# Kernel tuning notes

Measured on AMD Instinct MI355X. Metric: run time of the kernel, lower is better.

The kernel has to match this reference:

```python
import jax, jax.numpy as jnp
import numpy as np

DEPTH = 9                 # complete binary tree depth
N = 2 ** (DEPTH + 1) - 1  # 1023 nodes per tree (heap layout)
B = 32                    # batch of trees
E = 256                   # word_emb_dims
H = 512                   # treelstm in_dim (cell hidden size)
L = 512                   # decoder LSTM dims
V = 32000                 # vocab size
T = 64                    # max_sequence_length (greedy decode steps)


def setup_inputs() -> dict:
    key = jax.random.key(0)
    ks = jax.random.split(key, 12)
    g = lambda i, shape, s=0.02: jax.random.normal(ks[i], shape, jnp.float32) * s
    return {
        "node_feat": jax.random.randint(ks[0], (B, N), 0, V),
        "mask": jnp.ones((B, N), jnp.int32),
        # shared token embedding (node_emb_layer token_emb, also used by decoder input)
        "emb": g(1, (V, E)),
        # ChildSumTreeLSTMCell params (DGL convention)
        "W_iou": g(2, (E, 3 * H)),
        "U_iou": g(3, (H, 3 * H)),
        "b_iou": jnp.zeros((3 * H,), jnp.float32),
        "U_f_w": g(4, (H, H)),
        "U_f_b": jnp.zeros((H,), jnp.float32),
        # graph-readout -> decoder init state projections
        "hid_fc_w": g(5, (H, L)), "hid_fc_b": jnp.zeros((L,), jnp.float32),
        "cell_fc_w": g(6, (H, L)), "cell_fc_b": jnp.zeros((L,), jnp.float32),
        # decoder LSTMCell (PyTorch gate order i,f,g,o) + vocab projection
        "W_ih": g(7, (E, 4 * L)), "W_hh": g(8, (L, 4 * L)),
        "b_ih": jnp.zeros((4 * L,), jnp.float32), "b_hh": jnp.zeros((4 * L,), jnp.float32),
        "fc_w": g(9, (L, V)), "fc_b": jnp.zeros((V,), jnp.float32),
    }


def _forward(node_feat, mask, emb, W_iou, U_iou, b_iou, U_f_w, U_f_b,
             hid_fc_w, hid_fc_b, cell_fc_w, cell_fc_b,
             W_ih, W_hh, b_ih, b_hh, fc_w, fc_b):
    x = emb[node_feat]                                        # [B,N,E]
    iou_in = (x @ W_iou) * mask[..., None].astype(x.dtype)    # [B,N,3H]
    h = jnp.zeros((B, N, H), x.dtype)
    c = jnp.zeros((B, N, H), x.dtype)

    def apply_node(iou_node, c_agg):
        i, o, u = jnp.split(iou_node + b_iou, 3, axis=-1)
        i, o, u = jax.nn.sigmoid(i), jax.nn.sigmoid(o), jnp.tanh(u)
        c_new = i * u + c_agg
        return o * jnp.tanh(c_new), c_new

    # leaves first (no children -> zero aggregated cell)
    leaf = jnp.arange(2 ** DEPTH - 1, N)
    h_l, c_l = apply_node(iou_in[:, leaf], jnp.zeros((), x.dtype))
    h = h.at[:, leaf].set(h_l)
    c = c.at[:, leaf].set(c_l)

    # level-batched topological propagation (dgl.prop_nodes_topo)
    for d in range(DEPTH - 1, -1, -1):
        idx = jnp.arange(2 ** d - 1, 2 ** (d + 1) - 1)        # nodes at level d
        ch = jnp.stack([2 * idx + 1, 2 * idx + 2], axis=1)    # [n_d,2]
        h_ch, c_ch = h[:, ch], c[:, ch]                       # [B,n_d,2,H]
        h_tild = h_ch.sum(2)                                  # child-sum
        f = jax.nn.sigmoid(h_ch @ U_f_w + U_f_b)              # per-child forget gate
        c_agg = (f * c_ch).sum(2)
        h_n, c_n = apply_node(iou_in[:, idx] + h_tild @ U_iou, c_agg)
        h = h.at[:, idx].set(h_n)
        c = c.at[:, idx].set(c_n)

    mean_feats = h.mean(1)                                    # mean graph readout [B,H]
    hid = mean_feats @ hid_fc_w + hid_fc_b
    cel = mean_feats @ cell_fc_w + cell_fc_b

    def step(carry, _):
        inp, hs, cs = carry
        xt = emb[inp]                                         # [B,E]
        gates = xt @ W_ih + hs @ W_hh + b_ih + b_hh
        ig, fg, gg, og = jnp.split(gates, 4, axis=-1)
        cs = jax.nn.sigmoid(fg) * cs + jax.nn.sigmoid(ig) * jnp.tanh(gg)
        hs = jax.nn.sigmoid(og) * jnp.tanh(cs)
        logits = hs @ fc_w + fc_b                             # [B,V]
        top1 = jnp.argmax(logits, axis=-1)                    # greedy feedback
        return (top1, hs, cs), logits

    inp0 = jnp.zeros((B,), node_feat.dtype)
    _, logits_seq = jax.lax.scan(step, (inp0, hid, cel), None, length=T - 1)
    # t=0 row stays zeros, matching logits_output initialization
    return jnp.concatenate([jnp.zeros((1, B, V), x.dtype), logits_seq], axis=0)


def reference(node_feat, mask, emb, W_iou, U_iou, b_iou, U_f_w, U_f_b,
              hid_fc_w, hid_fc_b, cell_fc_w, cell_fc_b,
              W_ih, W_hh, b_ih, b_hh, fc_w, fc_b):
    return _forward(node_feat, mask, emb, W_iou, U_iou, b_iou, U_f_w, U_f_b,
                    hid_fc_w, hid_fc_b, cell_fc_w, cell_fc_b,
                    W_ih, W_hh, b_ih, b_hh, fc_w, fc_b)
```

## Files before the change

### kernel.cpp

```cpp
#include <hip/hip_runtime.h>
#include <math.h>

#define B_ 32
#define N_ 1023
#define E_ 256
#define H_ 512
#define V_ 32000
#define T_ 64
#define NBL 250

__device__ __forceinline__ float sigf(float x) { return 1.0f / (1.0f + expf(-x)); }

template<bool LEAF>
__global__ void __launch_bounds__(256)
iou_gemm_k(const int* __restrict__ node_feat, const int* __restrict__ mask,
           const float* __restrict__ emb, const float* __restrict__ Wiou,
           const float* __restrict__ Uiou, const float* __restrict__ hbuf,
           float* __restrict__ iou_out, int first, int n, int nshift)
{
    const int rows = B_ * n;
    const int K = LEAF ? E_ : (E_ + H_);
    const int rt = blockIdx.x, ct = blockIdx.y;
    const int tid = threadIdx.x;
    const int tr = tid >> 4, tc = tid & 15;

    __shared__ __align__(16) float As[8][136];
    __shared__ __align__(16) float Bs[8][136];

    float acc[8][8];
#pragma unroll
    for (int i = 0; i < 8; ++i)
#pragma unroll
        for (int j = 0; j < 8; ++j) acc[i][j] = 0.0f;

    const int lrow = tid >> 1;
    const int lkq  = (tid & 1) << 2;
    const int grow = rt * 128 + lrow;
    const bool rvalid = grow < rows;
    int tok = 0; float mval = 0.0f; int hoff1 = 0, hoff2 = 0;
    if (rvalid) {
        const int b = grow >> nshift, j = grow & (n - 1);
        const int node = first + j;
        tok  = node_feat[b * N_ + node];
        mval = (float)mask[b * N_ + node];
        if (!LEAF) {
            hoff1 = (b * N_ + 2 * node + 1) * H_;
            hoff2 = hoff1 + H_;
        }
    }
    const int bk   = tid >> 5;
    const int bcol = (tid & 31) << 2;
    const int gcol = ct * 128 + bcol;

    const int nkt = K >> 3;
    for (int kt = 0; kt < nkt; ++kt) {
        const int k0 = kt << 3;
        {
            const int kg = k0 + lkq;
            float4 v = make_float4(0.f, 0.f, 0.f, 0.f);
            if (rvalid) {
                if (LEAF || kg < E_) {
                    float4 e = *(const float4*)(emb + tok * E_ + kg);
                    v.x = e.x * mval; v.y = e.y * mval; v.z = e.z * mval; v.w = e.w * mval;
                } else {
                    const int kk = kg - E_;
                    float4 h1 = *(const float4*)(hbuf + hoff1 + kk);
                    float4 h2 = *(const float4*)(hbuf + hoff2 + kk);
                    v.x = h1.x + h2.x; v.y = h1.y + h2.y;
                    v.z = h1.z + h2.z; v.w = h1.w + h2.w;
                }
            }
            As[lkq + 0][lrow] = v.x;
            As[lkq + 1][lrow] = v.y;
            As[lkq + 2][lrow] = v.z;
            As[lkq + 3][lrow] = v.w;
        }
        {
            const int kg = k0 + bk;
            const float* src = (LEAF || kg < E_) ? (Wiou + kg * 1536 + gcol)
                                                 : (Uiou + (kg - E_) * 1536 + gcol);
            *(float4*)&Bs[bk][bcol] = *(const float4*)src;
        }
        __syncthreads();
#pragma unroll
        for (int kk = 0; kk < 8; ++kk) {
            float a[8], bb[8];
            *(float4*)&a[0]  = *(const float4*)&As[kk][tr << 3];
            *(float4*)&a[4]  = *(const float4*)&As[kk][(tr << 3) + 4];
            *(float4*)&bb[0] = *(const float4*)&Bs[kk][tc << 2];
            *(float4*)&bb[4] = *(const float4*)&Bs[kk][(tc << 2) + 64];
#pragma unroll
            for (int i = 0; i < 8; ++i)
#pragma unroll
                for (int j = 0; j < 8; ++j)
                    acc[i][j] = fmaf(a[i], bb[j], acc[i][j]);
        }
        __syncthreads();
    }
#pragma unroll
    for (int i = 0; i < 8; ++i) {
        const int r = rt * 128 + (tr << 3) + i;
        if (r < rows) {
            float* dst = iou_out + (size_t)r * 1536 + ct * 128;
            *(float4*)(dst + (tc << 2))      = make_float4(acc[i][0], acc[i][1], acc[i][2], acc[i][3]);
            *(float4*)(dst + 64 + (tc << 2)) = make_float4(acc[i][4], acc[i][5], acc[i][6], acc[i][7]);
        }
    }
}

__global__ void __launch_bounds__(256)
iou_small_k(const int* __restrict__ node_feat, const int* __restrict__ mask,
            const float* __restrict__ emb, const float* __restrict__ Wiou,
            const float* __restrict__ Uiou, const float* __restrict__ hbuf,
            float* __restrict__ iou_out, int first, int n, int nshift)
{
    const int rows = B_ * n;
    const int rt = blockIdx.x, ct = blockIdx.y;
    const int tid = threadIdx.x;
    const int tr = tid >> 4, tc = tid & 15;

    __shared__ __align__(16) float As[8][72];
    __shared__ __align__(16) float Bs[8][72];

    float acc[4][4];
#pragma unroll
    for (int i = 0; i < 4; ++i)
#pragma unroll
        for (int j = 0; j < 4; ++j) acc[i][j] = 0.0f;

    const int srow = tid & 63, skq = tid >> 6;
    const int grow = rt * 64 + srow;
    const bool rvalid = grow < rows;
    int tok = 0; float mval = 0.f; int hoff1 = 0, hoff2 = 0;
    if (rvalid) {
        const int b = grow >> nshift, j = grow & (n - 1);
        const int node = first + j;
        tok  = node_feat[b * N_ + node];
        mval = (float)mask[b * N_ + node];
        hoff1 = (b * N_ + 2 * node + 1) * H_;
        hoff2 = hoff1 + H_;
    }
    const int gcol = ct * 64 + srow;

    for (int kt = 0; kt < 96; ++kt) {
        const int k0 = kt << 3;
        {
            const int kg = k0 + (skq << 1);
            float2 v = make_float2(0.f, 0.f);
            if (rvalid) {
                if (kg < E_) {
                    float2 e = *(const float2*)(emb + tok * E_ + kg);
                    v.x = e.x * mval; v.y = e.y * mval;
                } else {
                    const int kk = kg - E_;
                    float2 h1 = *(const float2*)(hbuf + hoff1 + kk);
                    float2 h2 = *(const float2*)(hbuf + hoff2 + kk);
                    v.x = h1.x + h2.x; v.y = h1.y + h2.y;
                }
            }
            As[(skq << 1) + 0][srow] = v.x;
            As[(skq << 1) + 1][srow] = v.y;
        }
        {
            const int kg = k0 + (skq << 1);
            const float* s0 = (kg < E_) ? (Wiou + (size_t)kg * 1536 + gcol)
                                        : (Uiou + (size_t)(kg - E_) * 1536 + gcol);
            const float* s1 = ((kg + 1) < E_) ? (Wiou + (size_t)(kg + 1) * 1536 + gcol)
                                              : (Uiou + (size_t)(kg + 1 - E_) * 1536 + gcol);
            Bs[(skq << 1) + 0][srow] = *s0;
            Bs[(skq << 1) + 1][srow] = *s1;
        }
        __syncthreads();
#pragma unroll
        for (int kk = 0; kk < 8; ++kk) {
            float a[4], bb[4];
            *(float4*)&a[0]  = *(const float4*)&As[kk][tr << 2];
            *(float4*)&bb[0] = *(const float4*)&Bs[kk][tc << 2];
#pragma unroll
            for (int i = 0; i < 4; ++i)
#pragma unroll
                for (int j = 0; j < 4; ++j)
                    acc[i][j] = fmaf(a[i], bb[j], acc[i][j]);
        }
        __syncthreads();
    }
#pragma unroll
    for (int i = 0; i < 4; ++i) {
        const int r = rt * 64 + (tr << 2) + i;
        if (r < rows)
            *(float4*)(iou_out + (size_t)r * 1536 + ct * 64 + (tc << 2)) =
                make_float4(acc[i][0], acc[i][1], acc[i][2], acc[i][3]);
    }
}

__global__ void __launch_bounds__(256)
fagg_gemm_k(const float* __restrict__ hbuf, const float* __restrict__ cbuf,
            const float* __restrict__ Ufw, const float* __restrict__ Ufb,
            float* __restrict__ cagg, int first, int n, int nshift)
{
    const int rows = 64 * n;
    const int rt = blockIdx.x, ct = blockIdx.y;
    const int tid = threadIdx.x;
    const int tr = tid >> 4, tc = tid & 15;

    __shared__ __align__(16) float As[8][136];
    __shared__ __align__(16) float Bs[8][136];

    float acc[8][8];
#pragma unroll
    for (int i = 0; i < 8; ++i)
#pragma unroll
        for (int j = 0; j < 8; ++j) acc[i][j] = 0.0f;

    const int lrow = tid >> 1;
    const int lkq  = (tid & 1) << 2;
    const int grow = rt * 128 + lrow;
    const bool rvalid = grow < rows;
    int hoff = 0;
    if (rvalid) {
        const int bj = grow >> 1, s = grow & 1;
        const int b = bj >> nshift, j = bj & (n - 1);
        const int node = first + j;
        hoff = (b * N_ + 2 * node + 1 + s) * H_;
    }
    const int bk   = tid >> 5;
    const int bcol = (tid & 31) << 2;
    const int gcol = ct * 128 + bcol;

    for (int kt = 0; kt < 64; ++kt) {
        const int k0 = kt << 3;
        {
            const int kg = k0 + lkq;
            float4 v = make_float4(0.f, 0.f, 0.f, 0.f);
            if (rvalid) v = *(const float4*)(hbuf + hoff + kg);
            As[lkq + 0][lrow] = v.x;
            As[lkq + 1][lrow] = v.y;
            As[lkq + 2][lrow] = v.z;
            As[lkq + 3][lrow] = v.w;
        }
        {
            const int kg = k0 + bk;
            *(float4*)&Bs[bk][bcol] = *(const float4*)(Ufw + kg * H_ + gcol);
        }
        __syncthreads();
#pragma unroll
        for (int kk = 0; kk < 8; ++kk) {
            float a[8], bb[8];
            *(float4*)&a[0]  = *(const float4*)&As[kk][tr << 3];
            *(float4*)&a[4]  = *(const float4*)&As[kk][(tr << 3) + 4];
            *(float4*)&bb[0] = *(const float4*)&Bs[kk][tc << 2];
            *(float4*)&bb[4] = *(const float4*)&Bs[kk][(tc << 2) + 64];
#pragma unroll
            for (int i = 0; i < 8; ++i)
#pragma unroll
                for (int j = 0; j < 8; ++j)
                    acc[i][j] = fmaf(a[i], bb[j], acc[i][j]);
        }
        __syncthreads();
    }
#pragma unroll
    for (int p = 0; p < 4; ++p) {
        const int r0 = rt * 128 + (tr << 3) + 2 * p;
        if (r0 < rows) {
            const int bj = r0 >> 1;
            const int b = bj >> nshift, j = bj & (n - 1);
            const int node = first + j;
            const float* c1 = cbuf + (b * N_ + 2 * node + 1) * H_ + ct * 128;
            const float* c2 = c1 + H_;
            float* dst = cagg + bj * H_ + ct * 128;
#pragma unroll
            for (int g = 0; g < 2; ++g) {
                const int off = (g ? 64 : 0) + (tc << 2);
                const int jb = g * 4;
                float4 cc1 = *(const float4*)(c1 + off);
                float4 cc2 = *(const float4*)(c2 + off);
                float4 bbv = *(const float4*)(Ufb + ct * 128 + off);
                float4 res;
                res.x = sigf(acc[2*p][jb+0] + bbv.x) * cc1.x + sigf(acc[2*p+1][jb+0] + bbv.x) * cc2.x;
                res.y = sigf(acc[2*p][jb+1] + bbv.y) * cc1.y + sigf(acc[2*p+1][jb+1] + bbv.y) * cc2.y;
                res.z = sigf(acc[2*p][jb+2] + bbv.z) * cc1.z + sigf(acc[2*p+1][jb+2] + bbv.z) * cc2.z;
                res.w = sigf(acc[2*p][jb+3] + bbv.w) * cc1.w + sigf(acc[2*p+1][jb+3] + bbv.w) * cc2.w;
                *(float4*)(dst + off) = res;
            }
        }
    }
}

__global__ void __launch_bounds__(256)
fagg_small_k(const float* __restrict__ hbuf, const float* __restrict__ cbuf,
             const float* __restrict__ Ufw, const float* __restrict__ Ufb,
             float* __restrict__ cagg, int first, int n, int nshift)
{
    const int rows = 64 * n;
    const int rt = blockIdx.x, ct = blockIdx.y;
    const int tid = threadIdx.x;
    const int tr = tid >> 4, tc = tid & 15;

    __shared__ __align__(16) float As[8][72];
    __shared__ __align__(16) float Bs[8][72];

    float acc[4][4];
#pragma unroll
    for (int i = 0; i < 4; ++i)
#pragma unroll
        for (int j = 0; j < 4; ++j) acc[i][j] = 0.0f;

    const int srow = tid & 63, skq = tid >> 6;
    const int grow = rt * 64 + srow;
    const bool rvalid = grow < rows;
    int hoff = 0;
    if (rvalid) {
        const int bj = grow >> 1, s = grow & 1;
        const int b = bj >> nshift, j = bj & (n - 1);
        const int node = first + j;
        hoff = (b * N_ + 2 * node + 1 + s) * H_;
    }
    const int gcol = ct * 64 + srow;

    for (int kt = 0; kt < 64; ++kt) {
        const int k0 = kt << 3;
        {
            const int kg = k0 + (skq << 1);
            float2 v = make_float2(0.f, 0.f);
            if (rvalid) v = *(const float2*)(hbuf + hoff + kg);
            As[(skq << 1) + 0][srow] = v.x;
            As[(skq << 1) + 1][srow] = v.y;
        }
        {
            const int kg = k0 + (skq << 1);
            Bs[(skq << 1) + 0][srow] = Ufw[(size_t)kg * H_ + gcol];
            Bs[(skq << 1) + 1][srow] = Ufw[(size_t)(kg + 1) * H_ + gcol];
        }
        __syncthreads();
#pragma unroll
        for (int kk = 0; kk < 8; ++kk) {
            float a[4], bb[4];
            *(float4*)&a[0]  = *(const float4*)&As[kk][tr << 2];
            *(float4*)&bb[0] = *(const float4*)&Bs[kk][tc << 2];
#pragma unroll
            for (int i = 0; i < 4; ++i)
#pragma unroll
                for (int j = 0; j < 4; ++j)
                    acc[i][j] = fmaf(a[i], bb[j], acc[i][j]);
        }
        __syncthreads();
    }
#pragma unroll
    for (int p = 0; p < 2; ++p) {
        const int r0 = rt * 64 + (tr << 2) + 2 * p;
        if (r0 < rows) {
            const int bj = r0 >> 1;
            const int b = bj >> nshift, j = bj & (n - 1);
            const int node = first + j;
            const float* c1 = cbuf + (b * N_ + 2 * node + 1) * H_ + ct * 64;
            const float* c2 = c1 + H_;
            float* dst = cagg + bj * H_ + ct * 64;
            const int off = tc << 2;
            float4 cc1 = *(const float4*)(c1 + off);
            float4 cc2 = *(const float4*)(c2 + off);
            float4 bbv = *(const float4*)(Ufb + ct * 64 + off);
            float4 res;
            res.x = sigf(acc[2*p][0] + bbv.x) * cc1.x + sigf(acc[2*p+1][0] + bbv.x) * cc2.x;
            res.y = sigf(acc[2*p][1] + bbv.y) * cc1.y + sigf(acc[2*p+1][1] + bbv.y) * cc2.y;
            res.z = sigf(acc[2*p][2] + bbv.z) * cc1.z + sigf(acc[2*p+1][2] + bbv.z) * cc2.z;
            res.w = sigf(acc[2*p][3] + bbv.w) * cc1.w + sigf(acc[2*p+1][3] + bbv.w) * cc2.w;
            *(float4*)(dst + off) = res;
        }
    }
}

template<bool LEAF>
__global__ void apply_node_k(const float* __restrict__ iou,
                             const float* __restrict__ b_iou,
                             const float* __restrict__ cagg,
                             float* __restrict__ hbuf, float* __restrict__ cbuf,
                             int first, int n, int nshift)
{
    const int gid = blockIdx.x * 256 + threadIdx.x;
    if (gid >= B_ * n * 128) return;
    const int r = gid >> 7, col = (gid & 127) << 2;
    const float* row = iou + (size_t)r * 1536;
    float4 iv = *(const float4*)(row + col);
    float4 ov = *(const float4*)(row + 512 + col);
    float4 uv = *(const float4*)(row + 1024 + col);
    float4 bi = *(const float4*)(b_iou + col);
    float4 bo = *(const float4*)(b_iou + 512 + col);
    float4 bu = *(const float4*)(b_iou + 1024 + col);
    float4 ca = make_float4(0.f, 0.f, 0.f, 0.f);
    if (!LEAF) ca = *(const float4*)(cagg + r * H_ + col);
    float4 cn, hn;
    cn.x = sigf(iv.x + bi.x) * tanhf(uv.x + bu.x) + ca.x;
    cn.y = sigf(iv.y + bi.y) * tanhf(uv.y + bu.y) + ca.y;
    cn.z = sigf(iv.z + bi.z) * tanhf(uv.z + bu.z) + ca.z;
    cn.w = sigf(iv.w + bi.w) * tanhf(uv.w + bu.w) + ca.w;
    hn.x = sigf(ov.x + bo.x) * tanhf(cn.x);
    hn.y = sigf(ov.y + bo.y) * tanhf(cn.y);
    hn.z = sigf(ov.z + bo.z) * tanhf(cn.z);
    hn.w = sigf(ov.w + bo.w) * tanhf(cn.w);
    const int b = r >> nshift, j = r & (n - 1);
    const int node = first + j;
    const size_t o = (size_t)(b * N_ + node) * H_ + col;
    *(float4*)(cbuf + o) = cn;
    *(float4*)(hbuf + o) = hn;
}

__global__ void mean_part_k(const float* __restrict__ hbuf, float* __restrict__ mpart)
{
    const int bid = blockIdx.x;
    const int b = bid >> 3, chunk = bid & 7;
    const int tid = threadIdx.x;
    const int n0 = chunk * 128;
    const int n1 = (n0 + 128 < N_) ? (n0 + 128) : N_;
    float s0 = 0.f, s1 = 0.f;
    for (int nn = n0; nn < n1; ++nn) {
        const float* p = hbuf + (size_t)(b * N_ + nn) * H_;
        s0 += p[tid];
        s1 += p[tid + 256];
    }
    mpart[(bid << 9) + tid]       = s0;
    mpart[(bid << 9) + tid + 256] = s1;
}

__global__ void mean_fin_k(const float* __restrict__ mpart, float* __restrict__ mf)
{
    const int gid = blockIdx.x * 256 + threadIdx.x;
    const int b = gid >> 9, k = gid & 511;
    float s = 0.f;
#pragma unroll
    for (int c = 0; c < 8; ++c) s += mpart[(((b << 3) + c) << 9) + k];
    mf[gid] = s * (1.0f / 1023.0f);
}

__global__ void hidcel_k(const float* __restrict__ mf,
                         const float* __restrict__ hw, const float* __restrict__ hb,
                         const float* __restrict__ cw, const float* __restrict__ cb,
                         float* __restrict__ hs0, float* __restrict__ cs)
{
    const int gid = blockIdx.x * 256 + threadIdx.x;
    const int which = gid >> 14;
    const int b = (gid >> 9) & 31, l = gid & 511;
    const float* W = which ? cw : hw;
    float acc = which ? cb[l] : hb[l];
#pragma unroll 8
    for (int k = 0; k < H_; ++k) acc = fmaf(mf[b * H_ + k], W[k * H_ + l], acc);
    if (which) cs[b * H_ + l] = acc; else hs0[b * H_ + l] = acc;
}

__global__ void __launch_bounds__(256)
lstm_step_k(const float* __restrict__ emb, const float* __restrict__ W_ih,
            const float* __restrict__ W_hh, const float* __restrict__ b_ih,
            const float* __restrict__ b_hh, const float* __restrict__ pval,
            const int* __restrict__ pidx, const float* __restrict__ hs_in,
            float* __restrict__ hs_out, float* __restrict__ cs, int t)
{
    __shared__ __align__(16) float xh[768][9];
    __shared__ __align__(16) float part[4][8][8][4];
    __shared__ float rv[256];
    __shared__ int   ri[256];
    __shared__ int   tokS[8];
    const int tid = threadIdx.x;
    const int bg  = blockIdx.y;

    if (t == 1) {
        if (tid < 8) tokS[tid] = 0;
    } else {
        const int bs = tid >> 5, th = tid & 31;
        const int b = bg * 8 + bs;
        float bv = -INFINITY; int bi = 0x7fffffff;
        for (int p = th; p < NBL; p += 32) {
            const float v = pval[b * NBL + p];
            const int  ix = pidx[b * NBL + p];
            if (v > bv || (v == bv && ix < bi)) { bv = v; bi = ix; }
        }
        rv[tid] = bv; ri[tid] = bi;
        __syncthreads();
        if (tid < 8) {
            float Bv = -INFINITY; int Bi = 0x7fffffff;
#pragma unroll
            for (int c = 0; c < 32; ++c) {
                const float v = rv[tid * 32 + c];
                const int  ix = ri[tid * 32 + c];
                if (v > Bv || (v == Bv && ix < Bi)) { Bv = v; Bi = ix; }
            }
            tokS[tid] = Bi;
        }
    }
    __syncthreads();

#pragma unroll
    for (int b = 0; b < 8; ++b) {
        const int tok = tokS[b];
        xh[tid][b] = emb[(size_t)tok * E_ + tid];
        for (int k = tid; k < H_; k += 256)
            xh[E_ + k][b] = hs_in[(bg * 8 + b) * H_ + k];
    }
    __syncthreads();

    const int ks = tid >> 6;
    const int lane = tid & 63;
    const int bi = lane >> 3, li = lane & 7;
    const int l = blockIdx.x * 8 + li;
    float ai = 0.f, af = 0.f, ag = 0.f, ao = 0.f;
    const int k0 = ks * 192;
    for (int kk = 0; kk < 192; ++kk) {
        const int k = k0 + kk;
        const float xv = xh[k][bi];
        const float* p = (k < E_) ? (W_ih + (size_t)k * 2048 + l)
                                  : (W_hh + (size_t)(k - E_) * 2048 + l);
        ai = fmaf(xv, p[0],    ai);
        af = fmaf(xv, p[512],  af);
        ag = fmaf(xv, p[1024], ag);
        ao = fmaf(xv, p[1536], ao);
    }
    part[ks][bi][li][0] = ai;
    part[ks][bi][li][1] = af;
    part[ks][bi][li][2] = ag;
    part[ks][bi][li][3] = ao;
    __syncthreads();

    if (tid < 64) {
        const int b2 = tid >> 3, l2i = tid & 7;
        const int l2 = blockIdx.x * 8 + l2i;
        const int b = bg * 8 + b2;
        float s0 = 0.f, s1 = 0.f, s2 = 0.f, s3 = 0.f;
#pragma unroll
        for (int q = 0; q < 4; ++q) {
            s0 += part[q][b2][l2i][0];
            s1 += part[q][b2][l2i][1];
            s2 += part[q][b2][l2i][2];
            s3 += part[q][b2][l2i][3];
        }
        const float gi = s0 + b_ih[l2]        + b_hh[l2];
        const float gf = s1 + b_ih[512 + l2]  + b_hh[512 + l2];
        const float gg = s2 + b_ih[1024 + l2] + b_hh[1024 + l2];
        const float go = s3 + b_ih[1536 + l2] + b_hh[1536 + l2];
        const float co = cs[b * H_ + l2];
        const float cn = sigf(gf) * co + sigf(gi) * tanhf(gg);
        cs[b * H_ + l2] = cn;
        hs_out[b * H_ + l2] = sigf(go) * tanhf(cn);
    }
}

__global__ void __launch_bounds__(256)
logits_part_k(const float* __restrict__ fc_w, const float* __restrict__ hs,
              float* __restrict__ partial)
{
    __shared__ __align__(16) float sm[128 * 36];
    const int tid = threadIdx.x;
    const int blk = blockIdx.x;
    const int kq  = blockIdx.y;

    for (int idx = tid; idx < B_ * 128; idx += 256) {
        const int b = idx & 31, k = idx >> 5;
        sm[k * 36 + b] = hs[b * H_ + kq * 128 + k];
    }
    __syncthreads();

    const int w8   = (tid >> 6) << 3;
    const int lane = tid & 63;
    const int col  = (blk << 7) + (lane << 1);

    float acc[8][2];
#pragma unroll
    for (int i = 0; i < 8; ++i) { acc[i][0] = 0.f; acc[i][1] = 0.f; }

    const float* wp = fc_w + (size_t)(kq * 128) * V_ + col;
    const float* hp = sm + w8;
    float2 wreg[8];
#pragma unroll
    for (int j = 0; j < 8; ++j) wreg[j] = *(const float2*)(wp + (size_t)j * V_);
    for (int kb = 0; kb < 16; ++kb) {
        float2 wnxt[8];
        if (kb < 15) {
            const float* wq = wp + (size_t)((kb + 1) << 3) * V_;
#pragma unroll
            for (int j = 0; j < 8; ++j) wnxt[j] = *(const float2*)(wq + (size_t)j * V_);
        }
#pragma unroll
        for (int j = 0; j < 8; ++j) {
            const float* hq = hp + ((kb << 3) + j) * 36;
            float hv[8];
            *(float4*)&hv[0] = *(const float4*)(hq);
            *(float4*)&hv[4] = *(const float4*)(hq + 4);
#pragma unroll
            for (int i = 0; i < 8; ++i) {
                acc[i][0] = fmaf(hv[i], wreg[j].x, acc[i][0]);
                acc[i][1] = fmaf(hv[i], wreg[j].y, acc[i][1]);
            }
        }
        if (kb < 15) {
#pragma unroll
            for (int j = 0; j < 8; ++j) wreg[j] = wnxt[j];
        }
    }
#pragma unroll
    for (int i = 0; i < 8; ++i) {
        float* dst = partial + (size_t)(kq * B_ + w8 + i) * V_ + col;
        *(float2*)dst = make_float2(acc[i][0], acc[i][1]);
    }
}

__global__ void __launch_bounds__(256)
logits_fin_k(const float* __restrict__ partial, const float* __restrict__ fc_b,
             float* __restrict__ out_t, float* __restrict__ pval,
             int* __restrict__ pidx)
{
    __shared__ float rv[256];
    __shared__ int   ri[256];
    const int tid = threadIdx.x, blk = blockIdx.x;
    const int b = tid >> 3, cg = (tid & 7) << 4;
    const int colbase = (blk << 7) + cg;

    const float* p0 = partial + (size_t)b * V_ + colbase;
    const float* p1 = partial + (size_t)(B_ + b) * V_ + colbase;
    const float* p2 = partial + (size_t)(2 * B_ + b) * V_ + colbase;
    const float* p3 = partial + (size_t)(3 * B_ + b) * V_ + colbase;
    const float* bp = fc_b + colbase;
    float* op = out_t + (size_t)b * V_ + colbase;

    float bv = -INFINITY; int bi = 0;
#pragma unroll
    for (int q = 0; q < 4; ++q) {
        float4 a0 = *(const float4*)(p0 + (q << 2));
        float4 a1 = *(const float4*)(p1 + (q << 2));
        float4 a2 = *(const float4*)(p2 + (q << 2));
        float4 a3 = *(const float4*)(p3 + (q << 2));
        float4 d  = *(const float4*)(bp + (q << 2));
        float4 v;
        v.x = a0.x + a1.x + a2.x + a3.x + d.x;
        v.y = a0.y + a1.y + a2.y + a3.y + d.y;
        v.z = a0.z + a1.z + a2.z + a3.z + d.z;
        v.w = a0.w + a1.w + a2.w + a3.w + d.w;
        *(float4*)(op + (q << 2)) = v;
        const int c0 = cg + (q << 2);
        if (v.x > bv) { bv = v.x; bi = c0 + 0; }
        if (v.y > bv) { bv = v.y; bi = c0 + 1; }
        if (v.z > bv) { bv = v.z; bi = c0 + 2; }
        if (v.w > bv) { bv = v.w; bi = c0 + 3; }
    }
    rv[tid] = bv; ri[tid] = bi;
    __syncthreads();
    if (tid < B_) {
        float Bv = -INFINITY; int Bi = 0;
#pragma unroll
        for (int q = 0; q < 8; ++q) {
            const float v = rv[(tid << 3) + q];
            if (v > Bv) { Bv = v; Bi = ri[(tid << 3) + q]; }
        }
        pval[tid * NBL + blk] = Bv;
        pidx[tid * NBL + blk] = (blk << 7) + Bi;
    }
}

extern "C" void kernel_launch(void* const* d_in, const int* in_sizes, int n_in,
                              void* d_out, int out_size, void* d_ws, size_t ws_size,
                              hipStream_t stream)
{
    (void)in_sizes; (void)n_in; (void)out_size; (void)ws_size;
    const int*   node_feat = (const int*)  d_in[0];
    const int*   mask      = (const int*)  d_in[1];
    const float* emb       = (const float*)d_in[2];
    const float* W_iou     = (const float*)d_in[3];
    const float* U_iou     = (const float*)d_in[4];
    const float* b_iou     = (const float*)d_in[5];
    const float* U_f_w     = (const float*)d_in[6];
    const float* U_f_b     = (const float*)d_in[7];
    const float* hid_fc_w  = (const float*)d_in[8];
    const float* hid_fc_b  = (const float*)d_in[9];
    const float* cell_fc_w = (const float*)d_in[10];
    const float* cell_fc_b = (const float*)d_in[11];
    const float* W_ih      = (const float*)d_in[12];
    const float* W_hh      = (const float*)d_in[13];
    const float* b_ih      = (const float*)d_in[14];
    const float* b_hh      = (const float*)d_in[15];
    const float* fc_w      = (const float*)d_in[16];
    const float* fc_b      = (const float*)d_in[17];
    float* out = (float*)d_out;

    float* ws      = (float*)d_ws;
    float* iou_buf = ws;
    float* cagg    = ws + 12582912;
    float* hbuf    = ws + 16777216;
    float* cbuf    = ws + 33538048;
    float* mf      = ws + 50298880;
    float* hsb     = ws + 50315264;
    float* csb     = ws + 50348032;
    float* pval    = ws + 50364416;
    int*   pidx    = (int*)(ws + 50372416);
    float* mpart   = iou_buf;
    float* partial = iou_buf + 262144;

    for (int chunk = 0; chunk < 2; ++chunk) {
        const int first = 511 + 256 * chunk;
        dim3 g(64, 12);
        iou_gemm_k<true><<<g, 256, 0, stream>>>(node_feat, mask, emb, W_iou, U_iou,
                                                hbuf, iou_buf, first, 256, 8);
        apply_node_k<true><<<4096, 256, 0, stream>>>(iou_buf, b_iou, cagg,
                                                     hbuf, cbuf, first, 256, 8);
    }
    for (int d = 8; d >= 0; --d) {
        const int n = 1 << d, first = n - 1;
        if (n <= 64) {
            dim3 gf((64 * n + 63) / 64, 8);
            fagg_small_k<<<gf, 256, 0, stream>>>(hbuf, cbuf, U_f_w, U_f_b, cagg, first, n, d);
            dim3 gi((32 * n + 63) / 64, 24);
            iou_small_k<<<gi, 256, 0, stream>>>(node_feat, mask, emb, W_iou, U_iou,
                                                hbuf, iou_buf, first, n, d);
        } else {
            dim3 gf((64 * n + 127) / 128, 4);
            fagg_gemm_k<<<gf, 256, 0, stream>>>(hbuf, cbuf, U_f_w, U_f_b, cagg, first, n, d);
            dim3 gi((32 * n + 127) / 128, 12);
            iou_gemm_k<false><<<gi, 256, 0, stream>>>(node_feat, mask, emb, W_iou, U_iou,
                                                      hbuf, iou_buf, first, n, d);
        }
        apply_node_k<false><<<16 * n, 256, 0, stream>>>(iou_buf, b_iou, cagg,
                                                        hbuf, cbuf, first, n, d);
    }
    mean_part_k<<<256, 256, 0, stream>>>(hbuf, mpart);
    mean_fin_k<<<64, 256, 0, stream>>>(mpart, mf);
    hidcel_k<<<128, 256, 0, stream>>>(mf, hid_fc_w, hid_fc_b, cell_fc_w, cell_fc_b, hsb, csb);
    hipMemsetAsync(d_out, 0, (size_t)B_ * V_ * sizeof(float), stream);
    for (int t = 1; t < T_; ++t) {
        const float* hs_in  = hsb + ((t - 1) & 1) * (B_ * H_);
        float*       hs_out = hsb + (t & 1) * (B_ * H_);
        dim3 gl(64, 4);
        lstm_step_k<<<gl, 256, 0, stream>>>(emb, W_ih, W_hh, b_ih, b_hh,
                                            pval, pidx, hs_in, hs_out, csb, t);
        dim3 gp(NBL, 4);
        logits_part_k<<<gp, 256, 0, stream>>>(fc_w, hs_out, partial);
        logits_fin_k<<<NBL, 256, 0, stream>>>(partial, fc_b,
                                              out + (size_t)t * B_ * V_, pval, pidx);
    }
}
```

Before: 6.997 ms.

## Prefetch GEMM tiles into registers and fuse logits reduction via last-block atomic

The iou and forget-gate GEMM kernels now load the next K-tile into registers while computing on the current shared-memory tile, which hides global load latency at the cost of an extra barrier per iteration. The logits partial and finalize kernels are merged into one launch: the K split drops from 4 to 2, and the last block to finish each column tile, found through an atomic counter, adds the partials, adds the bias and computes the argmax. This removes one kernel launch and one partial-buffer pass per decode step. In exchange it adds fences and atomics, a per-step flag memset, and less parallelism in the vocab projection.

```diff
diff --git a/kernel.cpp b/kernel.cpp
--- a/kernel.cpp
+++ b/kernel.cpp
@@ -53,35 +53,57 @@
     const int gcol = ct * 128 + bcol;
 
     const int nkt = K >> 3;
+
+    {
+        float4 v = make_float4(0.f, 0.f, 0.f, 0.f);
+        if (rvalid) {
+            const int kg = lkq;
+            if (LEAF || kg < E_) {
+                float4 e = *(const float4*)(emb + tok * E_ + kg);
+                v.x = e.x * mval; v.y = e.y * mval; v.z = e.z * mval; v.w = e.w * mval;
+            } else {
+                const int kk = kg - E_;
+                float4 h1 = *(const float4*)(hbuf + hoff1 + kk);
+                float4 h2 = *(const float4*)(hbuf + hoff2 + kk);
+                v.x = h1.x + h2.x; v.y = h1.y + h2.y;
+                v.z = h1.z + h2.z; v.w = h1.w + h2.w;
+            }
+        }
+        As[lkq + 0][lrow] = v.x;
+        As[lkq + 1][lrow] = v.y;
+        As[lkq + 2][lrow] = v.z;
+        As[lkq + 3][lrow] = v.w;
+        const int kg = bk;
+        const float* src = (LEAF || kg < E_) ? (Wiou + (size_t)kg * 1536 + gcol)
+                                             : (Uiou + (size_t)(kg - E_) * 1536 + gcol);
+        *(float4*)&Bs[bk][bcol] = *(const float4*)src;
+    }
+    __syncthreads();
+
     for (int kt = 0; kt < nkt; ++kt) {
-        const int k0 = kt << 3;
-        {
-            const int kg = k0 + lkq;
-            float4 v = make_float4(0.f, 0.f, 0.f, 0.f);
+        float4 nA = make_float4(0.f, 0.f, 0.f, 0.f);
+        float4 nB;
+        const bool more = (kt + 1 < nkt);
+        if (more) {
+            const int k0n = (kt + 1) << 3;
             if (rvalid) {
+                const int kg = k0n + lkq;
                 if (LEAF || kg < E_) {
                     float4 e = *(const float4*)(emb + tok * E_ + kg);
-                    v.x = e.x * mval; v.y = e.y * mval; v.z = e.z * mval; v.w = e.w * mval;
+                    nA.x = e.x * mval; nA.y = e.y * mval; nA.z = e.z * mval; nA.w = e.w * mval;
                 } else {
                     const int kk = kg - E_;
                     float4 h1 = *(const float4*)(hbuf + hoff1 + kk);
                     float4 h2 = *(const float4*)(hbuf + hoff2 + kk);
-                    v.x = h1.x + h2.x; v.y = h1.y + h2.y;
-                    v.z = h1.z + h2.z; v.w = h1.w + h2.w;
+                    nA.x = h1.x + h2.x; nA.y = h1.y + h2.y;
+                    nA.z = h1.z + h2.z; nA.w = h1.w + h2.w;
                 }
             }
-            As[lkq + 0][lrow] = v.x;
-            As[lkq + 1][lrow] = v.y;
-            As[lkq + 2][lrow] = v.z;
-            As[lkq + 3][lrow] = v.w;
-        }
-        {
-            const int kg = k0 + bk;
-            const float* src = (LEAF || kg < E_) ? (Wiou + kg * 1536 + gcol)
-                                                 : (Uiou + (kg - E_) * 1536 + gcol);
-            *(float4*)&Bs[bk][bcol] = *(const float4*)src;
-        }
-        __syncthreads();
+            const int kg = k0n + bk;
+            const float* src = (LEAF || kg < E_) ? (Wiou + (size_t)kg * 1536 + gcol)
+                                                 : (Uiou + (size_t)(kg - E_) * 1536 + gcol);
+            nB = *(const float4*)src;
+        }
 #pragma unroll
         for (int kk = 0; kk < 8; ++kk) {
             float a[8], bb[8];
@@ -94,6 +116,14 @@
 #pragma unroll
                 for (int j = 0; j < 8; ++j)
                     acc[i][j] = fmaf(a[i], bb[j], acc[i][j]);
+        }
+        __syncthreads();
+        if (more) {
+            As[lkq + 0][lrow] = nA.x;
+            As[lkq + 1][lrow] = nA.y;
+            As[lkq + 2][lrow] = nA.z;
+            As[lkq + 3][lrow] = nA.w;
+            *(float4*)&Bs[bk][bcol] = nB;
         }
         __syncthreads();
     }
@@ -227,22 +257,26 @@
     const int bcol = (tid & 31) << 2;
     const int gcol = ct * 128 + bcol;
 
+    {
+        float4 v = make_float4(0.f, 0.f, 0.f, 0.f);
+        if (rvalid) v = *(const float4*)(hbuf + hoff + lkq);
+        As[lkq + 0][lrow] = v.x;
+        As[lkq + 1][lrow] = v.y;
+        As[lkq + 2][lrow] = v.z;
+        As[lkq + 3][lrow] = v.w;
+        *(float4*)&Bs[bk][bcol] = *(const float4*)(Ufw + (size_t)bk * H_ + gcol);
+    }
+    __syncthreads();
+
     for (int kt = 0; kt < 64; ++kt) {
-        const int k0 = kt << 3;
-        {
-            const int kg = k0 + lkq;
-            float4 v = make_float4(0.f, 0.f, 0.f, 0.f);
-            if (rvalid) v = *(const float4*)(hbuf + hoff + kg);
-            As[lkq + 0][lrow] = v.x;
-            As[lkq + 1][lrow] = v.y;
-            As[lkq + 2][lrow] = v.z;
-            As[lkq + 3][lrow] = v.w;
-        }
-        {
-            const int kg = k0 + bk;
-            *(float4*)&Bs[bk][bcol] = *(const float4*)(Ufw + kg * H_ + gcol);
-        }
-        __syncthreads();
+        float4 nA = make_float4(0.f, 0.f, 0.f, 0.f);
+        float4 nB;
+        const bool more = (kt + 1 < 64);
+        if (more) {
+            const int k0n = (kt + 1) << 3;
+            if (rvalid) nA = *(const float4*)(hbuf + hoff + k0n + lkq);
+            nB = *(const float4*)(Ufw + (size_t)(k0n + bk) * H_ + gcol);
+        }
 #pragma unroll
         for (int kk = 0; kk < 8; ++kk) {
             float a[8], bb[8];
@@ -255,6 +289,14 @@
 #pragma unroll
                 for (int j = 0; j < 8; ++j)
                     acc[i][j] = fmaf(a[i], bb[j], acc[i][j]);
+        }
+        __syncthreads();
+        if (more) {
+            As[lkq + 0][lrow] = nA.x;
+            As[lkq + 1][lrow] = nA.y;
+            As[lkq + 2][lrow] = nA.z;
+            As[lkq + 3][lrow] = nA.w;
+            *(float4*)&Bs[bk][bcol] = nB;
         }
         __syncthreads();
     }
@@ -542,17 +584,22 @@
 }
 
 __global__ void __launch_bounds__(256)
-logits_part_k(const float* __restrict__ fc_w, const float* __restrict__ hs,
-              float* __restrict__ partial)
-{
-    __shared__ __align__(16) float sm[128 * 36];
+logits_k(const float* __restrict__ fc_w, const float* __restrict__ fc_b,
+         const float* __restrict__ hs, float* __restrict__ partial,
+         float* __restrict__ out_t, float* __restrict__ pval,
+         int* __restrict__ pidx, int* __restrict__ flags)
+{
+    __shared__ __align__(16) float sm[256 * 36];
+    __shared__ float rv[256];
+    __shared__ int   ri[256];
+    __shared__ int   amFin;
     const int tid = threadIdx.x;
     const int blk = blockIdx.x;
-    const int kq  = blockIdx.y;
-
-    for (int idx = tid; idx < B_ * 128; idx += 256) {
+    const int kh  = blockIdx.y;
+
+    for (int idx = tid; idx < B_ * 256; idx += 256) {
         const int b = idx & 31, k = idx >> 5;
-        sm[k * 36 + b] = hs[b * H_ + kq * 128 + k];
+        sm[k * 36 + b] = hs[b * H_ + kh * 256 + k];
     }
     __syncthreads();
 
@@ -564,14 +611,14 @@
 #pragma unroll
     for (int i = 0; i < 8; ++i) { acc[i][0] = 0.f; acc[i][1] = 0.f; }
 
-    const float* wp = fc_w + (size_t)(kq * 128) * V_ + col;
+    const float* wp = fc_w + (size_t)(kh * 256) * V_ + col;
     const float* hp = sm + w8;
     float2 wreg[8];
 #pragma unroll
     for (int j = 0; j < 8; ++j) wreg[j] = *(const float2*)(wp + (size_t)j * V_);
-    for (int kb = 0; kb < 16; ++kb) {
+    for (int kb = 0; kb < 32; ++kb) {
         float2 wnxt[8];
-        if (kb < 15) {
+        if (kb < 31) {
             const float* wq = wp + (size_t)((kb + 1) << 3) * V_;
 #pragma unroll
             for (int j = 0; j < 8; ++j) wnxt[j] = *(const float2*)(wq + (size_t)j * V_);
@@ -588,49 +635,43 @@
                 acc[i][1] = fmaf(hv[i], wreg[j].y, acc[i][1]);
             }
         }
-        if (kb < 15) {
+        if (kb < 31) {
 #pragma unroll
             for (int j = 0; j < 8; ++j) wreg[j] = wnxt[j];
         }
     }
 #pragma unroll
     for (int i = 0; i < 8; ++i) {
-        float* dst = partial + (size_t)(kq * B_ + w8 + i) * V_ + col;
+        float* dst = partial + (size_t)(kh * B_ + w8 + i) * V_ + col;
         *(float2*)dst = make_float2(acc[i][0], acc[i][1]);
     }
-}
-
-__global__ void __launch_bounds__(256)
-logits_fin_k(const float* __restrict__ partial, const float* __restrict__ fc_b,
-             float* __restrict__ out_t, float* __restrict__ pval,
-             int* __restrict__ pidx)
-{
-    __shared__ float rv[256];
-    __shared__ int   ri[256];
-    const int tid = threadIdx.x, blk = blockIdx.x;
+
+    __threadfence();
+    if (tid == 0) {
+        const int old = __hip_atomic_fetch_add(&flags[blk], 1, __ATOMIC_ACQ_REL,
+                                               __HIP_MEMORY_SCOPE_AGENT);
+        amFin = (old == 1);
+    }
+    __syncthreads();
+    if (!amFin) return;
+    __threadfence();
+
     const int b = tid >> 3, cg = (tid & 7) << 4;
     const int colbase = (blk << 7) + cg;
-
     const float* p0 = partial + (size_t)b * V_ + colbase;
     const float* p1 = partial + (size_t)(B_ + b) * V_ + colbase;
-    const float* p2 = partial + (size_t)(2 * B_ + b) * V_ + colbase;
-    const float* p3 = partial + (size_t)(3 * B_ + b) * V_ + colbase;
     const float* bp = fc_b + colbase;
     float* op = out_t + (size_t)b * V_ + colbase;
 
     float bv = -INFINITY; int bi = 0;
 #pragma unroll
     for (int q = 0; q < 4; ++q) {
-        float4 a0 = *(const float4*)(p0 + (q << 2));
-        float4 a1 = *(const float4*)(p1 + (q << 2));
-        float4 a2 = *(const float4*)(p2 + (q << 2));
-        float4 a3 = *(const float4*)(p3 + (q << 2));
-        float4 d  = *(const float4*)(bp + (q << 2));
+        float4 a = *(const float4*)(p0 + (q << 2));
+        float4 c = *(const float4*)(p1 + (q << 2));
+        float4 d = *(const float4*)(bp + (q << 2));
         float4 v;
-        v.x = a0.x + a1.x + a2.x + a3.x + d.x;
-        v.y = a0.y + a1.y + a2.y + a3.y + d.y;
-        v.z = a0.z + a1.z + a2.z + a3.z + d.z;
-        v.w = a0.w + a1.w + a2.w + a3.w + d.w;
+        v.x = a.x + c.x + d.x; v.y = a.y + c.y + d.y;
+        v.z = a.z + c.z + d.z; v.w = a.w + c.w + d.w;
         *(float4*)(op + (q << 2)) = v;
         const int c0 = cg + (q << 2);
         if (v.x > bv) { bv = v.x; bi = c0 + 0; }
@@ -688,6 +729,7 @@
     float* pval    = ws + 50364416;
     int*   pidx    = (int*)(ws + 50372416);
     float* mpart   = iou_buf;
+    int*   flags   = (int*)(iou_buf + 131072);
     float* partial = iou_buf + 262144;
 
     for (int chunk = 0; chunk < 2; ++chunk) {
@@ -720,15 +762,16 @@
     mean_fin_k<<<64, 256, 0, stream>>>(mpart, mf);
     hidcel_k<<<128, 256, 0, stream>>>(mf, hid_fc_w, hid_fc_b, cell_fc_w, cell_fc_b, hsb, csb);
     hipMemsetAsync(d_out, 0, (size_t)B_ * V_ * sizeof(float), stream);
+    hipMemsetAsync(flags, 0, 16384 * sizeof(int), stream);
     for (int t = 1; t < T_; ++t) {
         const float* hs_in  = hsb + ((t - 1) & 1) * (B_ * H_);
         float*       hs_out = hsb + (t & 1) * (B_ * H_);
         dim3 gl(64, 4);
         lstm_step_k<<<gl, 256, 0, stream>>>(emb, W_ih, W_hh, b_ih, b_hh,
                                             pval, pidx, hs_in, hs_out, csb, t);
-        dim3 gp(NBL, 4);
-        logits_part_k<<<gp, 256, 0, stream>>>(fc_w, hs_out, partial);
-        logits_fin_k<<<NBL, 256, 0, stream>>>(partial, fc_b,
-                                              out + (size_t)t * B_ * V_, pval, pidx);
-    }
-}
+        dim3 gp(NBL, 2);
+        logits_k<<<gp, 256, 0, stream>>>(fc_w, fc_b, hs_out, partial,
+                                         out + (size_t)t * B_ * V_, pval, pidx,
+                                         flags + (t - 1) * 256);
+    }
+}
```

Measured after the change: 12.50 ms. 78.7% more time.

## Transpose decoder LSTM weights once and halve logits K-split partials

Applied to the files above, without the earlier changes.

Adds a one-time kernel that transposes W_ih/W_hh into a gate-major [2048][768] buffer so each LSTM step thread reads contiguous float4 weight rows, and changes the shared-memory x/h staging to a batch-major layout to match. Separately, the vocab projection now splits K into 2 halves instead of 4, so each block accumulates 256 rows and the finalize kernel sums two partial buffers instead of four. This is meant to cut uncoalesced strided weight loads and partial-sum traffic per decode step. The cost is half as many logits blocks (less parallelism) and a longer serial K loop per block.

```diff
diff --git a/kernel.cpp b/kernel.cpp
--- a/kernel.cpp
+++ b/kernel.cpp
@@ -447,13 +447,34 @@
 }
 
 __global__ void __launch_bounds__(256)
-lstm_step_k(const float* __restrict__ emb, const float* __restrict__ W_ih,
-            const float* __restrict__ W_hh, const float* __restrict__ b_ih,
-            const float* __restrict__ b_hh, const float* __restrict__ pval,
-            const int* __restrict__ pidx, const float* __restrict__ hs_in,
-            float* __restrict__ hs_out, float* __restrict__ cs, int t)
-{
-    __shared__ __align__(16) float xh[768][9];
+wtrans_k(const float* __restrict__ W_ih, const float* __restrict__ W_hh,
+         float* __restrict__ Wt)
+{
+    __shared__ float t[64][33];
+    const int k0 = blockIdx.x * 32;
+    const int g0 = blockIdx.y * 64;
+    const int tid = threadIdx.x;
+    for (int idx = tid; idx < 2048; idx += 256) {
+        const int kk = idx >> 6, gg = idx & 63;
+        const int k = k0 + kk;
+        t[gg][kk] = (k < E_) ? W_ih[(size_t)k * 2048 + g0 + gg]
+                             : W_hh[(size_t)(k - E_) * 2048 + g0 + gg];
+    }
+    __syncthreads();
+    for (int idx = tid; idx < 2048; idx += 256) {
+        const int gg = idx >> 5, kk = idx & 31;
+        Wt[(size_t)(g0 + gg) * 768 + k0 + kk] = t[gg][kk];
+    }
+}
+
+__global__ void __launch_bounds__(256)
+lstm_step_k(const float* __restrict__ emb, const float* __restrict__ Wt,
+            const float* __restrict__ b_ih, const float* __restrict__ b_hh,
+            const float* __restrict__ pval, const int* __restrict__ pidx,
+            const float* __restrict__ hs_in, float* __restrict__ hs_out,
+            float* __restrict__ cs, int t)
+{
+    __shared__ __align__(16) float xh[8][776];
     __shared__ __align__(16) float part[4][8][8][4];
     __shared__ float rv[256];
     __shared__ int   ri[256];
@@ -487,12 +508,13 @@
     }
     __syncthreads();
 
-#pragma unroll
-    for (int b = 0; b < 8; ++b) {
-        const int tok = tokS[b];
-        xh[tid][b] = emb[(size_t)tok * E_ + tid];
-        for (int k = tid; k < H_; k += 256)
-            xh[E_ + k][b] = hs_in[(bg * 8 + b) * H_ + k];
+    for (int idx = tid; idx < 8 * E_; idx += 256) {
+        const int b = idx >> 8, k = idx & 255;
+        xh[b][k] = emb[(size_t)tokS[b] * E_ + k];
+    }
+    for (int idx = tid; idx < 8 * H_; idx += 256) {
+        const int b = idx >> 9, k = idx & 511;
+        xh[b][E_ + k] = hs_in[(size_t)(bg * 8 + b) * H_ + k];
     }
     __syncthreads();
 
@@ -502,15 +524,26 @@
     const int l = blockIdx.x * 8 + li;
     float ai = 0.f, af = 0.f, ag = 0.f, ao = 0.f;
     const int k0 = ks * 192;
-    for (int kk = 0; kk < 192; ++kk) {
-        const int k = k0 + kk;
-        const float xv = xh[k][bi];
-        const float* p = (k < E_) ? (W_ih + (size_t)k * 2048 + l)
-                                  : (W_hh + (size_t)(k - E_) * 2048 + l);
-        ai = fmaf(xv, p[0],    ai);
-        af = fmaf(xv, p[512],  af);
-        ag = fmaf(xv, p[1024], ag);
-        ao = fmaf(xv, p[1536], ao);
+    const float* wi = Wt + (size_t)(l)        * 768 + k0;
+    const float* wf = Wt + (size_t)(512 + l)  * 768 + k0;
+    const float* wg = Wt + (size_t)(1024 + l) * 768 + k0;
+    const float* wo = Wt + (size_t)(1536 + l) * 768 + k0;
+    const float* xp = &xh[bi][k0];
+#pragma unroll 4
+    for (int kk = 0; kk < 192; kk += 4) {
+        const float4 xv = *(const float4*)(xp + kk);
+        const float4 w0 = *(const float4*)(wi + kk);
+        const float4 w1 = *(const float4*)(wf + kk);
+        const float4 w2 = *(const float4*)(wg + kk);
+        const float4 w3 = *(const float4*)(wo + kk);
+        ai = fmaf(xv.x, w0.x, ai); ai = fmaf(xv.y, w0.y, ai);
+        ai = fmaf(xv.z, w0.z, ai); ai = fmaf(xv.w, w0.w, ai);
+        af = fmaf(xv.x, w1.x, af); af = fmaf(xv.y, w1.y, af);
+        af = fmaf(xv.z, w1.z, af); af = fmaf(xv.w, w1.w, af);
+        ag = fmaf(xv.x, w2.x, ag); ag = fmaf(xv.y, w2.y, ag);
+        ag = fmaf(xv.z, w2.z, ag); ag = fmaf(xv.w, w2.w, ag);
+        ao = fmaf(xv.x, w3.x, ao); ao = fmaf(xv.y, w3.y, ao);
+        ao = fmaf(xv.z, w3.z, ao); ao = fmaf(xv.w, w3.w, ao);
     }
     part[ks][bi][li][0] = ai;
     part[ks][bi][li][1] = af;
@@ -545,14 +578,14 @@
 logits_part_k(const float* __restrict__ fc_w, const float* __restrict__ hs,
               float* __restrict__ partial)
 {
-    __shared__ __align__(16) float sm[128 * 36];
+    __shared__ __align__(16) float sm[256 * 36];
     const int tid = threadIdx.x;
     const int blk = blockIdx.x;
-    const int kq  = blockIdx.y;
-
-    for (int idx = tid; idx < B_ * 128; idx += 256) {
+    const int kh  = blockIdx.y;
+
+    for (int idx = tid; idx < B_ * 256; idx += 256) {
         const int b = idx & 31, k = idx >> 5;
-        sm[k * 36 + b] = hs[b * H_ + kq * 128 + k];
+        sm[k * 36 + b] = hs[b * H_ + kh * 256 + k];
     }
     __syncthreads();
 
@@ -564,14 +597,14 @@
 #pragma unroll
     for (int i = 0; i < 8; ++i) { acc[i][0] = 0.f; acc[i][1] = 0.f; }
 
-    const float* wp = fc_w + (size_t)(kq * 128) * V_ + col;
+    const float* wp = fc_w + (size_t)(kh * 256) * V_ + col;
     const float* hp = sm + w8;
     float2 wreg[8];
 #pragma unroll
     for (int j = 0; j < 8; ++j) wreg[j] = *(const float2*)(wp + (size_t)j * V_);
-    for (int kb = 0; kb < 16; ++kb) {
+    for (int kb = 0; kb < 32; ++kb) {
         float2 wnxt[8];
-        if (kb < 15) {
+        if (kb < 31) {
             const float* wq = wp + (size_t)((kb + 1) << 3) * V_;
 #pragma unroll
             for (int j = 0; j < 8; ++j) wnxt[j] = *(const float2*)(wq + (size_t)j * V_);
@@ -588,14 +621,14 @@
                 acc[i][1] = fmaf(hv[i], wreg[j].y, acc[i][1]);
             }
         }
-        if (kb < 15) {
+        if (kb < 31) {
 #pragma unroll
             for (int j = 0; j < 8; ++j) wreg[j] = wnxt[j];
         }
     }
 #pragma unroll
     for (int i = 0; i < 8; ++i) {
-        float* dst = partial + (size_t)(kq * B_ + w8 + i) * V_ + col;
+        float* dst = partial + (size_t)(kh * B_ + w8 + i) * V_ + col;
         *(float2*)dst = make_float2(acc[i][0], acc[i][1]);
     }
 }
@@ -613,24 +646,18 @@
 
     const float* p0 = partial + (size_t)b * V_ + colbase;
     const float* p1 = partial + (size_t)(B_ + b) * V_ + colbase;
-    const float* p2 = partial + (size_t)(2 * B_ + b) * V_ + colbase;
-    const float* p3 = partial + (size_t)(3 * B_ + b) * V_ + colbase;
     const float* bp = fc_b + colbase;
     float* op = out_t + (size_t)b * V_ + colbase;
 
     float bv = -INFINITY; int bi = 0;
 #pragma unroll
     for (int q = 0; q < 4; ++q) {
-        float4 a0 = *(const float4*)(p0 + (q << 2));
-        float4 a1 = *(const float4*)(p1 + (q << 2));
-        float4 a2 = *(const float4*)(p2 + (q << 2));
-        float4 a3 = *(const float4*)(p3 + (q << 2));
-        float4 d  = *(const float4*)(bp + (q << 2));
+        float4 a = *(const float4*)(p0 + (q << 2));
+        float4 c = *(const float4*)(p1 + (q << 2));
+        float4 d = *(const float4*)(bp + (q << 2));
         float4 v;
-        v.x = a0.x + a1.x + a2.x + a3.x + d.x;
-        v.y = a0.y + a1.y + a2.y + a3.y + d.y;
-        v.z = a0.z + a1.z + a2.z + a3.z + d.z;
-        v.w = a0.w + a1.w + a2.w + a3.w + d.w;
+        v.x = a.x + c.x + d.x; v.y = a.y + c.y + d.y;
+        v.z = a.z + c.z + d.z; v.w = a.w + c.w + d.w;
         *(float4*)(op + (q << 2)) = v;
         const int c0 = cg + (q << 2);
         if (v.x > bv) { bv = v.x; bi = c0 + 0; }
@@ -689,6 +716,7 @@
     int*   pidx    = (int*)(ws + 50372416);
     float* mpart   = iou_buf;
     float* partial = iou_buf + 262144;
+    float* Wt      = iou_buf + 2359296;
 
     for (int chunk = 0; chunk < 2; ++chunk) {
         const int first = 511 + 256 * chunk;
@@ -719,14 +747,16 @@
     mean_part_k<<<256, 256, 0, stream>>>(hbuf, mpart);
     mean_fin_k<<<64, 256, 0, stream>>>(mpart, mf);
     hidcel_k<<<128, 256, 0, stream>>>(mf, hid_fc_w, hid_fc_b, cell_fc_w, cell_fc_b, hsb, csb);
+    dim3 gw(24, 32);
+    wtrans_k<<<gw, 256, 0, stream>>>(W_ih, W_hh, Wt);
     hipMemsetAsync(d_out, 0, (size_t)B_ * V_ * sizeof(float), stream);
     for (int t = 1; t < T_; ++t) {
         const float* hs_in  = hsb + ((t - 1) & 1) * (B_ * H_);
         float*       hs_out = hsb + (t & 1) * (B_ * H_);
         dim3 gl(64, 4);
-        lstm_step_k<<<gl, 256, 0, stream>>>(emb, W_ih, W_hh, b_ih, b_hh,
+        lstm_step_k<<<gl, 256, 0, stream>>>(emb, Wt, b_ih, b_hh,
                                             pval, pidx, hs_in, hs_out, csb, t);
-        dim3 gp(NBL, 4);
+        dim3 gp(NBL, 2);
         logits_part_k<<<gp, 256, 0, stream>>>(fc_w, hs_out, partial);
         logits_fin_k<<<NBL, 256, 0, stream>>>(partial, fc_b,
                                               out + (size_t)t * B_ * V_, pval, pidx);
```

New measurement: 5.996 ms. -14.3%, faster.
